# Optimization experiments

Hardware: AMD Instinct MI355X
Metric: run time of the kernel (lower is better)

## Reference

```python
import jax, jax.numpy as jnp
import numpy as np


def _proj(x, w, b):
    # 1x1 conv as channel matmul: x (n,c,h,w), w (k,c), b (k,) -> (n,k,h,w)
    return jnp.einsum('nchw,kc->nkhw', x, w) + b[None, :, None, None]


def setup_inputs() -> dict:
    key = jax.random.key(0)
    ks = jax.random.split(key, 9)
    cin, cinter = 256, 128
    n, h, w = 4, 64, 64
    s = lambda fan_in: 1.0 / np.sqrt(fan_in)
    return {
        'x': jax.random.normal(ks[0], (n, cin, h, w), jnp.float32),
        'theta_w': jax.random.normal(ks[1], (cinter, cin), jnp.float32) * s(cin),
        'theta_b': jax.random.normal(ks[2], (cinter,), jnp.float32) * 0.01,
        'phi_w': jax.random.normal(ks[3], (cinter, cin), jnp.float32) * s(cin),
        'phi_b': jax.random.normal(ks[4], (cinter,), jnp.float32) * 0.01,
        'g_w': jax.random.normal(ks[5], (cinter, cin), jnp.float32) * s(cin),
        'g_b': jax.random.normal(ks[6], (cinter,), jnp.float32) * 0.01,
        'w_w': jax.random.normal(ks[7], (cin, cinter), jnp.float32) * s(cinter),
        'w_b': jax.random.normal(ks[8], (cin,), jnp.float32) * 0.01,
    }


def reference(x, theta_w, theta_b, phi_w, phi_b, g_w, g_b, w_w, w_b):
    n, c, h, w = x.shape
    cinter = theta_w.shape[0]
    hw = h * w
    theta_x = _proj(x, theta_w, theta_b).reshape(n, cinter, hw)  # (n,ci,HW)
    phi_x = _proj(x, phi_w, phi_b).reshape(n, cinter, hw)        # (n,ci,HW)
    g_x = _proj(x, g_w, g_b).reshape(n, cinter, hw)              # (n,ci,HW)
    # f_x = phi^T @ theta : (n, HW, HW), softmax over last dim (theta positions)
    f_x = jnp.einsum('nci,ncj->nij', phi_x, theta_x)
    f_x = jax.nn.softmax(f_x, axis=-1)
    # attended = g @ f : (n, ci, HW)
    att = jnp.einsum('nci,nij->ncj', g_x, f_x).reshape(n, cinter, h, w)
    res_x = _proj(att, w_w, w_b)  # (n, c, h, w)
    return x + res_x
```

## Files before the change

kernel.cpp:

```cpp
#include <hip/hip_runtime.h>
#include <hip/hip_bf16.h>

#define B_ 4
#define C_ 256
#define CI_ 128
#define P_ 4096
#define LOG2E 1.44269504088896340736f

typedef __attribute__((ext_vector_type(8))) _Float16 half8;
typedef __attribute__((ext_vector_type(2))) __fp16 fp16x2;
typedef __attribute__((ext_vector_type(8))) short short8;
typedef __attribute__((ext_vector_type(4))) short short4v;
typedef __attribute__((ext_vector_type(4))) float floatx4;

__device__ __forceinline__ float bf2f(ushort h) {
  union { unsigned u; float f; } v; v.u = ((unsigned)h) << 16; return v.f;
}
__device__ __forceinline__ ushort f2bf(float f) {
  union { float f; unsigned u; } v; v.f = f;
  unsigned r = v.u + 0x7FFFu + ((v.u >> 16) & 1u);
  return (ushort)(r >> 16);
}
__device__ __forceinline__ ushort f2h(float f) {
  _Float16 h = (_Float16)f;
  union { _Float16 h; ushort u; } v; v.h = h; return v.u;
}
__device__ __forceinline__ uint2 pk4h(float a, float b, float c, float d) {
  union { fp16x2 h[2]; uint2 u; } pk;
  pk.h[0] = __builtin_amdgcn_cvt_pkrtz(a, b);
  pk.h[1] = __builtin_amdgcn_cvt_pkrtz(c, d);
  return pk.u;
}

#define MFMA16(a, b, c) __builtin_amdgcn_mfma_f32_16x16x32_f16((a), (b), (c), 0, 0, 0)

__device__ __forceinline__ int detect_bf16(const ushort* __restrict__ xu) {
  __shared__ int cnt_;
  if (threadIdx.x == 0) cnt_ = 0;
  __syncthreads();
  int local = 0;
  int t = threadIdx.x & 255;
#pragma unroll
  for (int s = 0; s < 8; ++s) {
    ushort u = xu[(t * 8 + s) * 2];
    int e = (u >> 7) & 0xFF;
    local += (e >= 0x70 && e <= 0x84) ? 1 : 0;
  }
  atomicAdd(&cnt_, local);
  __syncthreads();
  return cnt_ > 1024;
}

__global__ void k_trc(const void* __restrict__ xv, ushort* __restrict__ xT,
                      const void* __restrict__ s0, const void* __restrict__ s1,
                      const void* __restrict__ s2, const void* __restrict__ s3,
                      const void* __restrict__ tbv, const void* __restrict__ pbv,
                      const void* __restrict__ gbv, const void* __restrict__ wbv,
                      ushort* __restrict__ dstW, float* __restrict__ biasf) {
  int is_bf16 = detect_bf16((const ushort*)xv);
  int bid = blockIdx.x;
  int t = threadIdx.x;
  if (bid < 1024) {
    __shared__ __align__(16) ushort tile[64][74];
    int pb = (bid & 63) * 64;
    int cb = ((bid >> 6) & 3) * 64;
    int b = bid >> 8;
#pragma unroll
    for (int it = 0; it < 2; ++it) {
      int lin = it * 256 + t;
      int c = lin >> 3;
      int p = (lin & 7) * 8;
      size_t base = ((size_t)(b * C_) + cb + c) * P_ + pb + p;
      float vv[8];
      if (is_bf16) {
        short8 v = *(const short8*)((const ushort*)xv + base);
#pragma unroll
        for (int i = 0; i < 8; ++i) vv[i] = bf2f((ushort)v[i]);
      } else {
        const float* xf = (const float*)xv;
        float4 v0 = *(const float4*)(xf + base);
        float4 v1 = *(const float4*)(xf + base + 4);
        vv[0] = v0.x; vv[1] = v0.y; vv[2] = v0.z; vv[3] = v0.w;
        vv[4] = v1.x; vv[5] = v1.y; vv[6] = v1.z; vv[7] = v1.w;
      }
#pragma unroll
      for (int i = 0; i < 8; ++i) {
        int iw = (i + t) & 7;
        tile[p + iw][c] = f2h(vv[iw]);
      }
    }
    __syncthreads();
#pragma unroll
    for (int it = 0; it < 2; ++it) {
      int lin = it * 256 + t;
      int p = lin >> 3;
      int c = (lin & 7) * 8;
      short8 v = *(const short8*)&tile[p][c];
      *(short8*)(xT + ((size_t)(b * P_) + pb + p) * C_ + cb + c) = v;
    }
  } else if (bid < 1536) {
    int wid = bid - 1024;
    int a = wid >> 7;
    const void* srcs[4] = {s0, s1, s2, s3};
    int i = (wid & 127) * 256 + t;
    float v = is_bf16 ? bf2f(((const ushort*)srcs[a])[i]) : ((const float*)srcs[a])[i];
    dstW[a * 32768 + i] = f2h(v);
  } else {
    int idx = (bid - 1536) * 256 + t;
    if (idx < 640) {
      const void* src; int loc;
      if (idx < 128)      { src = tbv; loc = idx; }
      else if (idx < 256) { src = pbv; loc = idx - 128; }
      else if (idx < 384) { src = gbv; loc = idx - 256; }
      else                { src = wbv; loc = idx - 384; }
      float v = is_bf16 ? bf2f(((const ushort*)src)[loc]) : ((const float*)src)[loc];
      biasf[idx] = v;
    }
  }
}

__global__ __launch_bounds__(256, 4) void k_proj(
    const ushort* __restrict__ xT, const ushort* __restrict__ Wh,
    const float* __restrict__ biasf,
    ushort* __restrict__ thetaT, ushort* __restrict__ phiT,
    ushort* __restrict__ g) {
  int t = threadIdx.x;
  int w = t >> 6, lane = t & 63, l = lane & 15, q = lane >> 4;
  int pblk = blockIdx.x * 32;
  int b = blockIdx.y;
  floatx4 acc[2][6];
#pragma unroll
  for (int ps = 0; ps < 2; ++ps)
#pragma unroll
    for (int ks = 0; ks < 6; ++ks) acc[ps][ks] = (floatx4){0.f, 0.f, 0.f, 0.f};
  const ushort* xrow[2];
#pragma unroll
  for (int ps = 0; ps < 2; ++ps)
    xrow[ps] = xT + ((size_t)(b * P_) + pblk + ps * 16 + l) * C_;
  const ushort* wrow[6];
  int prj[6], kloc[6];
#pragma unroll
  for (int ks = 0; ks < 6; ++ks) {
    int kg = w * 96 + ks * 16;
    prj[ks] = kg >> 7;
    kloc[ks] = kg & 127;
    wrow[ks] = Wh + prj[ks] * 32768 + (size_t)(kloc[ks] + l) * C_;
  }
  for (int c = 0; c < C_; c += 32) {
    half8 av[2], wv[6];
#pragma unroll
    for (int ps = 0; ps < 2; ++ps) av[ps] = *(const half8*)(xrow[ps] + c + q * 8);
#pragma unroll
    for (int ks = 0; ks < 6; ++ks) wv[ks] = *(const half8*)(wrow[ks] + c + q * 8);
#pragma unroll
    for (int ps = 0; ps < 2; ++ps)
#pragma unroll
      for (int ks = 0; ks < 6; ++ks)
        acc[ps][ks] = MFMA16(av[ps], wv[ks], acc[ps][ks]);
  }
#pragma unroll
  for (int ks = 0; ks < 6; ++ks) {
    float bias = biasf[prj[ks] * 128 + kloc[ks] + l];
#pragma unroll
    for (int ps = 0; ps < 2; ++ps) {
      floatx4 d = acc[ps][ks];
      if (prj[ks] < 2) {
        ushort* dst = (prj[ks] == 0 ? thetaT : phiT) +
                      ((size_t)(b * P_) + pblk + ps * 16 + q * 4) * CI_ + kloc[ks] + l;
#pragma unroll
        for (int r = 0; r < 4; ++r) dst[(size_t)r * CI_] = f2h(d[r] + bias);
      } else {
        ushort* dst = g + ((size_t)(b * CI_) + kloc[ks] + l) * P_ + pblk + ps * 16 + q * 4;
        short4v pk;
#pragma unroll
        for (int r = 0; r < 4; ++r) pk[r] = (short)f2h(d[r] + bias);
        *(short4v*)dst = pk;
      }
    }
  }
}

__global__ __launch_bounds__(256, 2) void k_stats(
    const ushort* __restrict__ phiT, const ushort* __restrict__ thetaT,
    float* __restrict__ part) {
  __shared__ __align__(16) ushort thS[2][32][138];
  int t = threadIdx.x, w = t >> 6, lane = t & 63, l = lane & 15, q = lane >> 4;
  int wgid = blockIdx.x;
  int xcd = wgid & 7, slot = wgid >> 3;
  int st = xcd + 8 * (slot >> 4);
  int i0 = (slot & 15) * 256;
  int jsp = st & 7;
  int j0 = jsp * 512;
  int b = st >> 3;
  const ushort* tb0 = thetaT + (size_t)b * P_ * CI_;
#pragma unroll
  for (int it = 0; it < 2; ++it) {
    int lin = it * 256 + t, row = lin >> 4, cg = (lin & 15) * 8;
    *(short8*)&thS[0][row][cg] = *(const short8*)(tb0 + (size_t)(j0 + row) * CI_ + cg);
  }
  half8 av[4][4];
#pragma unroll
  for (int is = 0; is < 4; ++is) {
    const ushort* pr = phiT + ((size_t)(b * P_) + i0 + w * 64 + is * 16 + l) * CI_;
#pragma unroll
    for (int ks = 0; ks < 4; ++ks) av[is][ks] = *(const half8*)(pr + ks * 32 + q * 8);
  }
  float sum[4][4];
#pragma unroll
  for (int is = 0; is < 4; ++is)
#pragma unroll
    for (int r = 0; r < 4; ++r) sum[is][r] = 0.f;
  __syncthreads();
  for (int jc = 0; jc < 16; ++jc) {
    if (jc < 15) {
      int jr = j0 + (jc + 1) * 32;
      int bufn = (jc + 1) & 1;
#pragma unroll
      for (int it = 0; it < 2; ++it) {
        int lin = it * 256 + t, row = lin >> 4, cg = (lin & 15) * 8;
        *(short8*)&thS[bufn][row][cg] =
            *(const short8*)(tb0 + (size_t)(jr + row) * CI_ + cg);
      }
    }
    int buf = jc & 1;
    half8 bv[2][4];
#pragma unroll
    for (int js = 0; js < 2; ++js)
#pragma unroll
      for (int ks = 0; ks < 4; ++ks)
        bv[js][ks] = *(const half8*)&thS[buf][js * 16 + l][ks * 32 + q * 8];
    floatx4 accS[4][2];
#pragma unroll
    for (int is = 0; is < 4; ++is)
#pragma unroll
      for (int js = 0; js < 2; ++js) accS[is][js] = (floatx4){0.f, 0.f, 0.f, 0.f};
#pragma unroll
    for (int ks = 0; ks < 4; ++ks)
#pragma unroll
      for (int is = 0; is < 4; ++is)
#pragma unroll
        for (int js = 0; js < 2; ++js)
          accS[is][js] = MFMA16(av[is][ks], bv[js][ks], accS[is][js]);
#pragma unroll
    for (int is = 0; is < 4; ++is)
#pragma unroll
      for (int js = 0; js < 2; ++js)
#pragma unroll
        for (int r = 0; r < 4; ++r)
          sum[is][r] += exp2f(fmaf(accS[is][js][r], LOG2E, -64.f));
    __syncthreads();
  }
#pragma unroll
  for (int d = 1; d < 16; d <<= 1)
#pragma unroll
    for (int is = 0; is < 4; ++is)
#pragma unroll
      for (int r = 0; r < 4; ++r) sum[is][r] += __shfl_xor(sum[is][r], d, 64);
  if (l == 0) {
#pragma unroll
    for (int is = 0; is < 4; ++is)
#pragma unroll
      for (int r = 0; r < 4; ++r)
        part[((size_t)jsp * B_ + b) * P_ + i0 + w * 64 + is * 16 + q * 4 + r] =
            sum[is][r];
  }
}

__global__ void k_lse(const float* __restrict__ part, float* __restrict__ o2) {
  int idx = blockIdx.x * 256 + threadIdx.x;
  float s = 0.f;
#pragma unroll
  for (int p = 0; p < 8; ++p) s += part[(size_t)p * (B_ * P_) + idx];
  o2[idx] = log2f(s) + 64.f;
}

__global__ __launch_bounds__(256, 2) void k_attn(
    const ushort* __restrict__ phiT, const ushort* __restrict__ thetaT,
    const ushort* __restrict__ g, const float* __restrict__ o2,
    ushort* __restrict__ attPA, ushort* __restrict__ attPB,
    int nIH, int nChunk) {
  __shared__ __align__(16) ushort thL[128][136];
  __shared__ __align__(16) ushort eL[128][136];
  int t = threadIdx.x;
  int w = t >> 6, lane = t & 63, l = lane & 15, q = lane >> 4;
  int wgid = blockIdx.x;
  int xcd = wgid & 7, slot = wgid >> 3;
  int st = xcd + 8 * (slot >> 5);
  int j0 = (slot & 31) * 128;
  int ih = st & (nIH - 1);
  int b = st >> ((nIH == 4) ? 2 : 1);
#pragma unroll
  for (int it = 0; it < 8; ++it) {
    int lin = it * 256 + t, row = lin >> 4, cg = (lin & 15) * 8;
    *(short8*)&thL[row][cg] =
        *(const short8*)(thetaT + ((size_t)(b * P_) + j0 + row) * CI_ + cg);
  }
  floatx4 accA[2][8];
#pragma unroll
  for (int cs = 0; cs < 2; ++cs)
#pragma unroll
    for (int js = 0; js < 8; ++js) accA[cs][js] = (floatx4){0.f, 0.f, 0.f, 0.f};
  const float* orow = o2 + b * P_;
  int istart = ih * nChunk * 128;
  half8 af[2][4];
  float ov[2][4];
  uint2 ep[2][8];
#pragma unroll
  for (int is = 0; is < 2; ++is) {
    int iG = istart + w * 32 + is * 16;
    const ushort* pr = phiT + ((size_t)(b * P_) + iG + l) * CI_;
#pragma unroll
    for (int ks = 0; ks < 4; ++ks) af[is][ks] = *(const half8*)(pr + ks * 32 + q * 8);
#pragma unroll
    for (int r = 0; r < 4; ++r) ov[is][r] = orow[iG + q * 4 + r];
  }
  __syncthreads();
#pragma unroll
  for (int js = 0; js < 8; ++js) {
    half8 bf[4];
#pragma unroll
    for (int ks = 0; ks < 4; ++ks)
      bf[ks] = *(const half8*)&thL[js * 16 + l][ks * 32 + q * 8];
#pragma unroll
    for (int is = 0; is < 2; ++is) {
      floatx4 s = (floatx4){0.f, 0.f, 0.f, 0.f};
#pragma unroll
      for (int ks = 0; ks < 4; ++ks) s = MFMA16(af[is][ks], bf[ks], s);
      float e0 = exp2f(fmaf(s[0], LOG2E, -ov[is][0]));
      float e1 = exp2f(fmaf(s[1], LOG2E, -ov[is][1]));
      float e2 = exp2f(fmaf(s[2], LOG2E, -ov[is][2]));
      float e3 = exp2f(fmaf(s[3], LOG2E, -ov[is][3]));
      ep[is][js] = pk4h(e0, e1, e2, e3);
    }
  }
  for (int ic = 0; ic < nChunk; ++ic) {
    int ibase = istart + ic * 128;
    half8 gf[2][4];
#pragma unroll
    for (int cs = 0; cs < 2; ++cs) {
      const ushort* gr = g + ((size_t)(b * CI_) + w * 32 + cs * 16 + l) * P_ + ibase;
#pragma unroll
      for (int ks = 0; ks < 4; ++ks) gf[cs][ks] = *(const half8*)(gr + ks * 32 + q * 8);
    }
    __syncthreads();
#pragma unroll
    for (int is = 0; is < 2; ++is)
#pragma unroll
      for (int js = 0; js < 8; ++js)
        *(uint2*)&eL[js * 16 + l][w * 32 + is * 16 + q * 4] = ep[is][js];
    __syncthreads();
    if (ic + 1 < nChunk) {
      int nb = istart + (ic + 1) * 128;
#pragma unroll
      for (int is = 0; is < 2; ++is) {
        int iG = nb + w * 32 + is * 16;
        const ushort* pr = phiT + ((size_t)(b * P_) + iG + l) * CI_;
#pragma unroll
        for (int ks = 0; ks < 4; ++ks) af[is][ks] = *(const half8*)(pr + ks * 32 + q * 8);
#pragma unroll
        for (int r = 0; r < 4; ++r) ov[is][r] = orow[iG + q * 4 + r];
      }
    }
    __builtin_amdgcn_s_setprio(1);
#pragma unroll
    for (int ks = 0; ks < 4; ++ks) {
      half8 ef[8];
#pragma unroll
      for (int js = 0; js < 8; ++js) ef[js] = *(const half8*)&eL[js * 16 + l][ks * 32 + q * 8];
#pragma unroll
      for (int cs = 0; cs < 2; ++cs)
#pragma unroll
        for (int js = 0; js < 8; ++js) accA[cs][js] = MFMA16(gf[cs][ks], ef[js], accA[cs][js]);
    }
    __builtin_amdgcn_s_setprio(0);
    if (ic + 1 < nChunk) {
#pragma unroll
      for (int js = 0; js < 8; ++js) {
        half8 bf[4];
#pragma unroll
        for (int ks = 0; ks < 4; ++ks)
          bf[ks] = *(const half8*)&thL[js * 16 + l][ks * 32 + q * 8];
#pragma unroll
        for (int is = 0; is < 2; ++is) {
          floatx4 s = (floatx4){0.f, 0.f, 0.f, 0.f};
#pragma unroll
          for (int ks = 0; ks < 4; ++ks) s = MFMA16(af[is][ks], bf[ks], s);
          float e0 = exp2f(fmaf(s[0], LOG2E, -ov[is][0]));
          float e1 = exp2f(fmaf(s[1], LOG2E, -ov[is][1]));
          float e2 = exp2f(fmaf(s[2], LOG2E, -ov[is][2]));
          float e3 = exp2f(fmaf(s[3], LOG2E, -ov[is][3]));
          ep[is][js] = pk4h(e0, e1, e2, e3);
        }
      }
    }
  }
  ushort* ap = (ih < 2 ? attPA : attPB) + (size_t)(ih & 1) * (B_ * P_ * CI_);
#pragma unroll
  for (int cs = 0; cs < 2; ++cs)
#pragma unroll
    for (int js = 0; js < 8; ++js) {
      uint2 pk = pk4h(accA[cs][js][0], accA[cs][js][1], accA[cs][js][2], accA[cs][js][3]);
      *(uint2*)(ap + ((size_t)(b * P_) + j0 + js * 16 + l) * CI_ +
                w * 32 + cs * 16 + q * 4) = pk;
    }
}

__global__ __launch_bounds__(256, 4) void k_out(
    const ushort* __restrict__ attPA, const ushort* __restrict__ attPB, int nIH,
    const ushort* __restrict__ wwh, const float* __restrict__ biasf,
    const void* __restrict__ xv, void* __restrict__ outv) {
  int is_bf16 = detect_bf16((const ushort*)xv);
  int t = threadIdx.x;
  int w = t >> 6, lane = t & 63, l = lane & 15, q = lane >> 4;
  int p0 = blockIdx.x * 32, b = blockIdx.y;
  floatx4 accR[4][2];
#pragma unroll
  for (int kk = 0; kk < 4; ++kk)
#pragma unroll
    for (int js = 0; js < 2; ++js) accR[kk][js] = (floatx4){0.f, 0.f, 0.f, 0.f};
#pragma unroll
  for (int ks = 0; ks < 4; ++ks) {
    half8 wf[4], af[2];
#pragma unroll
    for (int kk = 0; kk < 4; ++kk)
      wf[kk] = *(const half8*)(wwh + (size_t)(w * 64 + kk * 16 + l) * CI_ + ks * 32 + q * 8);
#pragma unroll
    for (int js = 0; js < 2; ++js) {
      size_t off = ((size_t)(b * P_) + p0 + js * 16 + l) * CI_ + ks * 32 + q * 8;
      half8 s = *(const half8*)(attPA + off);
      s = s + *(const half8*)(attPA + (size_t)(B_ * P_) * CI_ + off);
      if (nIH == 4) {
        s = s + *(const half8*)(attPB + off);
        s = s + *(const half8*)(attPB + (size_t)(B_ * P_) * CI_ + off);
      }
      af[js] = s;
    }
#pragma unroll
    for (int kk = 0; kk < 4; ++kk)
#pragma unroll
      for (int js = 0; js < 2; ++js) accR[kk][js] = MFMA16(wf[kk], af[js], accR[kk][js]);
  }
#pragma unroll
  for (int kk = 0; kk < 4; ++kk)
#pragma unroll
    for (int r = 0; r < 4; ++r) {
      int c = w * 64 + kk * 16 + q * 4 + r;
      float bias = biasf[384 + c];
#pragma unroll
      for (int js = 0; js < 2; ++js) {
        int p = p0 + js * 16 + l;
        size_t idx = ((size_t)(b * C_) + c) * P_ + p;
        float val = accR[kk][js][r] + bias;
        if (is_bf16) {
          ((ushort*)outv)[idx] = f2bf(bf2f(((const ushort*)xv)[idx]) + val);
        } else {
          ((float*)outv)[idx] = ((const float*)xv)[idx] + val;
        }
      }
    }
}

extern "C" void kernel_launch(void* const* d_in, const int* in_sizes, int n_in,
                              void* d_out, int out_size, void* d_ws, size_t ws_size,
                              hipStream_t stream) {
  const void* x  = d_in[0];
  const void* tw = d_in[1];
  const void* tb = d_in[2];
  const void* pw = d_in[3];
  const void* pb = d_in[4];
  const void* gw = d_in[5];
  const void* gb = d_in[6];
  const void* ww = d_in[7];
  const void* wb = d_in[8];
  char* ws = (char*)d_ws;
  float*  o2     = (float*)(ws);
  float*  part   = (float*)(ws + (64u << 10));
  ushort* Wh     = (ushort*)(ws + (576u << 10));
  float*  biasf  = (float*)(ws + (832u << 10));
  ushort* xT     = (ushort*)(ws + (1u << 20));
  ushort* attPA  = xT;
  ushort* thetaT = (ushort*)(ws + (9u << 20));
  ushort* phiT   = (ushort*)(ws + (13u << 20));
  ushort* gbuf   = (ushort*)(ws + (17u << 20));
  ushort* attPB  = (ushort*)(ws + (21u << 20));
  int big = (ws_size >= (30u << 20)) ? 1 : 0;

  k_trc<<<1539, 256, 0, stream>>>(x, xT, tw, pw, gw, ww, tb, pb, gb, wb, Wh, biasf);
  k_proj<<<dim3(128, 4), 256, 0, stream>>>(xT, Wh, biasf, thetaT, phiT, gbuf);
  k_stats<<<512, 256, 0, stream>>>(phiT, thetaT, part);
  k_lse<<<64, 256, 0, stream>>>(part, o2);
  if (big) {
    k_attn<<<512, 256, 0, stream>>>(phiT, thetaT, gbuf, o2, attPA, attPB, 4, 8);
    k_out<<<dim3(128, 4), 256, 0, stream>>>(attPA, attPB, 4, Wh + 3 * 32768, biasf, x, d_out);
  } else {
    k_attn<<<256, 256, 0, stream>>>(phiT, thetaT, gbuf, o2, attPA, attPB, 2, 16);
    k_out<<<dim3(128, 4), 256, 0, stream>>>(attPA, attPB, 2, Wh + 3 * 32768, biasf, x, d_out);
  }
}
```

Measured before the change: 220.8 us.

## Fuse x transpose into projection and replace LSE pass with atomic row sums

The standalone transpose of x into a half-precision xT buffer is removed. k_proj now loads its 32-position x tile straight from the input and transposes it through shared memory. The separate k_lse kernel is also dropped: k_stats atomically adds its partial exp sums into a zeroed sums buffer (cleared in k_trc), and k_attn computes log2 on the fly. This cuts one kernel launch plus a round trip of the transposed x through global memory, at the cost of atomics, strided uncoalesced-ish x loads and bf16 detection in k_proj, and nondeterministic summation order.

```diff
diff --git a/kernel.cpp b/kernel.cpp
--- a/kernel.cpp
+++ b/kernel.cpp
@@ -51,62 +51,24 @@
   return cnt_ > 1024;
 }
 
-__global__ void k_trc(const void* __restrict__ xv, ushort* __restrict__ xT,
+__global__ void k_trc(const void* __restrict__ xv,
                       const void* __restrict__ s0, const void* __restrict__ s1,
                       const void* __restrict__ s2, const void* __restrict__ s3,
                       const void* __restrict__ tbv, const void* __restrict__ pbv,
                       const void* __restrict__ gbv, const void* __restrict__ wbv,
-                      ushort* __restrict__ dstW, float* __restrict__ biasf) {
+                      ushort* __restrict__ dstW, float* __restrict__ biasf,
+                      float* __restrict__ sums) {
   int is_bf16 = detect_bf16((const ushort*)xv);
   int bid = blockIdx.x;
   int t = threadIdx.x;
-  if (bid < 1024) {
-    __shared__ __align__(16) ushort tile[64][74];
-    int pb = (bid & 63) * 64;
-    int cb = ((bid >> 6) & 3) * 64;
-    int b = bid >> 8;
-#pragma unroll
-    for (int it = 0; it < 2; ++it) {
-      int lin = it * 256 + t;
-      int c = lin >> 3;
-      int p = (lin & 7) * 8;
-      size_t base = ((size_t)(b * C_) + cb + c) * P_ + pb + p;
-      float vv[8];
-      if (is_bf16) {
-        short8 v = *(const short8*)((const ushort*)xv + base);
-#pragma unroll
-        for (int i = 0; i < 8; ++i) vv[i] = bf2f((ushort)v[i]);
-      } else {
-        const float* xf = (const float*)xv;
-        float4 v0 = *(const float4*)(xf + base);
-        float4 v1 = *(const float4*)(xf + base + 4);
-        vv[0] = v0.x; vv[1] = v0.y; vv[2] = v0.z; vv[3] = v0.w;
-        vv[4] = v1.x; vv[5] = v1.y; vv[6] = v1.z; vv[7] = v1.w;
-      }
-#pragma unroll
-      for (int i = 0; i < 8; ++i) {
-        int iw = (i + t) & 7;
-        tile[p + iw][c] = f2h(vv[iw]);
-      }
-    }
-    __syncthreads();
-#pragma unroll
-    for (int it = 0; it < 2; ++it) {
-      int lin = it * 256 + t;
-      int p = lin >> 3;
-      int c = (lin & 7) * 8;
-      short8 v = *(const short8*)&tile[p][c];
-      *(short8*)(xT + ((size_t)(b * P_) + pb + p) * C_ + cb + c) = v;
-    }
-  } else if (bid < 1536) {
-    int wid = bid - 1024;
-    int a = wid >> 7;
+  if (bid < 512) {
+    int a = bid >> 7;
     const void* srcs[4] = {s0, s1, s2, s3};
-    int i = (wid & 127) * 256 + t;
+    int i = (bid & 127) * 256 + t;
     float v = is_bf16 ? bf2f(((const ushort*)srcs[a])[i]) : ((const float*)srcs[a])[i];
     dstW[a * 32768 + i] = f2h(v);
-  } else {
-    int idx = (bid - 1536) * 256 + t;
+  } else if (bid < 515) {
+    int idx = (bid - 512) * 256 + t;
     if (idx < 640) {
       const void* src; int loc;
       if (idx < 128)      { src = tbv; loc = idx; }
@@ -116,27 +78,52 @@
       float v = is_bf16 ? bf2f(((const ushort*)src)[loc]) : ((const float*)src)[loc];
       biasf[idx] = v;
     }
+  } else {
+    int zi = (bid - 515) * 256 + t;
+    *(float4*)(sums + (size_t)zi * 4) = (float4){0.f, 0.f, 0.f, 0.f};
   }
 }
 
 __global__ __launch_bounds__(256, 4) void k_proj(
-    const ushort* __restrict__ xT, const ushort* __restrict__ Wh,
+    const void* __restrict__ xv, const ushort* __restrict__ Wh,
     const float* __restrict__ biasf,
     ushort* __restrict__ thetaT, ushort* __restrict__ phiT,
     ushort* __restrict__ g) {
+  __shared__ __align__(16) ushort xS[32][264];
+  int is_bf16 = detect_bf16((const ushort*)xv);
   int t = threadIdx.x;
   int w = t >> 6, lane = t & 63, l = lane & 15, q = lane >> 4;
   int pblk = blockIdx.x * 32;
   int b = blockIdx.y;
+#pragma unroll
+  for (int it = 0; it < 4; ++it) {
+    int lin = it * 256 + t;
+    int cc = lin >> 2;
+    int pp = (lin & 3) * 8;
+    size_t base = ((size_t)(b * C_) + cc) * P_ + pblk + pp;
+    float vv[8];
+    if (is_bf16) {
+      short8 v = *(const short8*)((const ushort*)xv + base);
+#pragma unroll
+      for (int i = 0; i < 8; ++i) vv[i] = bf2f((ushort)v[i]);
+    } else {
+      const float* xf = (const float*)xv;
+      float4 v0 = *(const float4*)(xf + base);
+      float4 v1 = *(const float4*)(xf + base + 4);
+      vv[0] = v0.x; vv[1] = v0.y; vv[2] = v0.z; vv[3] = v0.w;
+      vv[4] = v1.x; vv[5] = v1.y; vv[6] = v1.z; vv[7] = v1.w;
+    }
+#pragma unroll
+    for (int i = 0; i < 8; ++i) {
+      int iw = (i + t) & 7;
+      xS[pp + iw][cc] = f2h(vv[iw]);
+    }
+  }
   floatx4 acc[2][6];
 #pragma unroll
   for (int ps = 0; ps < 2; ++ps)
 #pragma unroll
     for (int ks = 0; ks < 6; ++ks) acc[ps][ks] = (floatx4){0.f, 0.f, 0.f, 0.f};
-  const ushort* xrow[2];
-#pragma unroll
-  for (int ps = 0; ps < 2; ++ps)
-    xrow[ps] = xT + ((size_t)(b * P_) + pblk + ps * 16 + l) * C_;
   const ushort* wrow[6];
   int prj[6], kloc[6];
 #pragma unroll
@@ -146,10 +133,11 @@
     kloc[ks] = kg & 127;
     wrow[ks] = Wh + prj[ks] * 32768 + (size_t)(kloc[ks] + l) * C_;
   }
+  __syncthreads();
   for (int c = 0; c < C_; c += 32) {
     half8 av[2], wv[6];
 #pragma unroll
-    for (int ps = 0; ps < 2; ++ps) av[ps] = *(const half8*)(xrow[ps] + c + q * 8);
+    for (int ps = 0; ps < 2; ++ps) av[ps] = *(const half8*)&xS[ps * 16 + l][c + q * 8];
 #pragma unroll
     for (int ks = 0; ks < 6; ++ks) wv[ks] = *(const half8*)(wrow[ks] + c + q * 8);
 #pragma unroll
@@ -182,7 +170,7 @@
 
 __global__ __launch_bounds__(256, 2) void k_stats(
     const ushort* __restrict__ phiT, const ushort* __restrict__ thetaT,
-    float* __restrict__ part) {
+    float* __restrict__ sums) {
   __shared__ __align__(16) ushort thS[2][32][138];
   int t = threadIdx.x, w = t >> 6, lane = t & 63, l = lane & 15, q = lane >> 4;
   int wgid = blockIdx.x;
@@ -261,22 +249,14 @@
     for (int is = 0; is < 4; ++is)
 #pragma unroll
       for (int r = 0; r < 4; ++r)
-        part[((size_t)jsp * B_ + b) * P_ + i0 + w * 64 + is * 16 + q * 4 + r] =
-            sum[is][r];
-  }
-}
-
-__global__ void k_lse(const float* __restrict__ part, float* __restrict__ o2) {
-  int idx = blockIdx.x * 256 + threadIdx.x;
-  float s = 0.f;
-#pragma unroll
-  for (int p = 0; p < 8; ++p) s += part[(size_t)p * (B_ * P_) + idx];
-  o2[idx] = log2f(s) + 64.f;
+        atomicAdd(&sums[(size_t)b * P_ + i0 + w * 64 + is * 16 + q * 4 + r],
+                  sum[is][r]);
+  }
 }
 
 __global__ __launch_bounds__(256, 2) void k_attn(
     const ushort* __restrict__ phiT, const ushort* __restrict__ thetaT,
-    const ushort* __restrict__ g, const float* __restrict__ o2,
+    const ushort* __restrict__ g, const float* __restrict__ sums,
     ushort* __restrict__ attPA, ushort* __restrict__ attPB,
     int nIH, int nChunk) {
   __shared__ __align__(16) ushort thL[128][136];
@@ -300,7 +280,7 @@
   for (int cs = 0; cs < 2; ++cs)
 #pragma unroll
     for (int js = 0; js < 8; ++js) accA[cs][js] = (floatx4){0.f, 0.f, 0.f, 0.f};
-  const float* orow = o2 + b * P_;
+  const float* srow = sums + b * P_;
   int istart = ih * nChunk * 128;
   half8 af[2][4];
   float ov[2][4];
@@ -311,8 +291,11 @@
     const ushort* pr = phiT + ((size_t)(b * P_) + iG + l) * CI_;
 #pragma unroll
     for (int ks = 0; ks < 4; ++ks) af[is][ks] = *(const half8*)(pr + ks * 32 + q * 8);
-#pragma unroll
-    for (int r = 0; r < 4; ++r) ov[is][r] = orow[iG + q * 4 + r];
+    float4 sv = *(const float4*)(srow + iG + q * 4);
+    ov[is][0] = log2f(sv.x) + 64.f;
+    ov[is][1] = log2f(sv.y) + 64.f;
+    ov[is][2] = log2f(sv.z) + 64.f;
+    ov[is][3] = log2f(sv.w) + 64.f;
   }
   __syncthreads();
 #pragma unroll
@@ -357,8 +340,11 @@
         const ushort* pr = phiT + ((size_t)(b * P_) + iG + l) * CI_;
 #pragma unroll
         for (int ks = 0; ks < 4; ++ks) af[is][ks] = *(const half8*)(pr + ks * 32 + q * 8);
-#pragma unroll
-        for (int r = 0; r < 4; ++r) ov[is][r] = orow[iG + q * 4 + r];
+        float4 sv = *(const float4*)(srow + iG + q * 4);
+        ov[is][0] = log2f(sv.x) + 64.f;
+        ov[is][1] = log2f(sv.y) + 64.f;
+        ov[is][2] = log2f(sv.z) + 64.f;
+        ov[is][3] = log2f(sv.w) + 64.f;
       }
     }
     __builtin_amdgcn_s_setprio(1);
@@ -473,27 +459,24 @@
   const void* ww = d_in[7];
   const void* wb = d_in[8];
   char* ws = (char*)d_ws;
-  float*  o2     = (float*)(ws);
-  float*  part   = (float*)(ws + (64u << 10));
+  float*  sums   = (float*)(ws);
   ushort* Wh     = (ushort*)(ws + (576u << 10));
   float*  biasf  = (float*)(ws + (832u << 10));
-  ushort* xT     = (ushort*)(ws + (1u << 20));
-  ushort* attPA  = xT;
+  ushort* attPA  = (ushort*)(ws + (1u << 20));
   ushort* thetaT = (ushort*)(ws + (9u << 20));
   ushort* phiT   = (ushort*)(ws + (13u << 20));
   ushort* gbuf   = (ushort*)(ws + (17u << 20));
   ushort* attPB  = (ushort*)(ws + (21u << 20));
   int big = (ws_size >= (30u << 20)) ? 1 : 0;
 
-  k_trc<<<1539, 256, 0, stream>>>(x, xT, tw, pw, gw, ww, tb, pb, gb, wb, Wh, biasf);
-  k_proj<<<dim3(128, 4), 256, 0, stream>>>(xT, Wh, biasf, thetaT, phiT, gbuf);
-  k_stats<<<512, 256, 0, stream>>>(phiT, thetaT, part);
-  k_lse<<<64, 256, 0, stream>>>(part, o2);
+  k_trc<<<531, 256, 0, stream>>>(x, tw, pw, gw, ww, tb, pb, gb, wb, Wh, biasf, sums);
+  k_proj<<<dim3(128, 4), 256, 0, stream>>>(x, Wh, biasf, thetaT, phiT, gbuf);
+  k_stats<<<512, 256, 0, stream>>>(phiT, thetaT, sums);
   if (big) {
-    k_attn<<<512, 256, 0, stream>>>(phiT, thetaT, gbuf, o2, attPA, attPB, 4, 8);
+    k_attn<<<512, 256, 0, stream>>>(phiT, thetaT, gbuf, sums, attPA, attPB, 4, 8);
     k_out<<<dim3(128, 4), 256, 0, stream>>>(attPA, attPB, 4, Wh + 3 * 32768, biasf, x, d_out);
   } else {
-    k_attn<<<256, 256, 0, stream>>>(phiT, thetaT, gbuf, o2, attPA, attPB, 2, 16);
+    k_attn<<<256, 256, 0, stream>>>(phiT, thetaT, gbuf, sums, attPA, attPB, 2, 16);
     k_out<<<dim3(128, 4), 256, 0, stream>>>(attPA, attPB, 2, Wh + 3 * 32768, biasf, x, d_out);
   }
 }
```

Measured after the change: 217.1 us, median of 3. No clear change (-1.7%).
